# Kernel tuning notes

Measured on AMD Instinct MI355X. Metric: run time of the kernel, lower is better.

Reference implementation:

```python
import jax, jax.numpy as jnp
import numpy as np

DIM = 128
NUM_HEADS = 4
WH, WW = 7, 7
N = WH * WW            # 49 tokens per window
NW = 64                # number of windows (56/7)^2
BATCH = 64
B_ = BATCH * NW        # 4096


def _relative_position_index(Wh, Ww):
    coords = np.stack(np.meshgrid(np.arange(Wh), np.arange(Ww), indexing='ij'))  # [2,Wh,Ww]
    coords = coords.reshape(2, -1)
    rel = coords[:, :, None] - coords[:, None, :]          # [2, N, N]
    rel = rel.transpose(1, 2, 0).astype(np.int64)          # [N, N, 2]
    rel[:, :, 0] += Wh - 1
    rel[:, :, 1] += Ww - 1
    rel[:, :, 0] *= 2 * Ww - 1
    return rel.sum(-1)                                     # [N, N]


def setup_inputs() -> dict:
    key = jax.random.key(0)
    ks = jax.random.split(key, 8)
    x = jax.random.normal(ks[0], (B_, N, DIM), dtype=jnp.float32)
    # Swin shift-mask: additive, 0 or large negative; random floats are fine for math check
    mask = jax.random.normal(ks[1], (NW, N, N), dtype=jnp.float32)
    qkv_w = jax.random.normal(ks[2], (DIM, 3 * DIM), dtype=jnp.float32) * 0.02
    qkv_b = jax.random.normal(ks[3], (3 * DIM,), dtype=jnp.float32) * 0.02
    proj_w = jax.random.normal(ks[4], (DIM, DIM), dtype=jnp.float32) * 0.02
    proj_b = jax.random.normal(ks[5], (DIM,), dtype=jnp.float32) * 0.02
    table_size = (2 * WH - 1) * (2 * WW - 1)  # 169
    bias_table = jax.random.normal(ks[6], (table_size, NUM_HEADS), dtype=jnp.float32) * 0.02
    rel_idx = jnp.asarray(_relative_position_index(WH, WW), dtype=jnp.int32)  # [N,N]
    return {"x": x, "mask": mask, "qkv_w": qkv_w, "qkv_b": qkv_b,
            "proj_w": proj_w, "proj_b": proj_b, "bias_table": bias_table,
            "rel_idx": rel_idx}


def reference(x, mask, qkv_w, qkv_b, proj_w, proj_b, bias_table, rel_idx):
    B, Nn, C = x.shape
    H = bias_table.shape[1]
    hd = C // H
    scale = hd ** -0.5
    # qkv projection -> [3, B, H, N, hd]
    qkv = (x @ qkv_w + qkv_b).reshape(B, Nn, 3, H, hd).transpose(2, 0, 3, 1, 4)
    q, k, v = qkv[0] * scale, qkv[1], qkv[2]
    attn = jnp.einsum('bhnd,bhmd->bhnm', q, k)  # [B,H,N,N]
    # gathered relative position bias -> [H,N,N]
    bias = bias_table[rel_idx.reshape(-1)].reshape(Nn, Nn, H).transpose(2, 0, 1)
    attn = attn + bias[None]
    nW = mask.shape[0]
    attn = attn.reshape(-1, nW, H, Nn, Nn) + mask[None, :, None].astype(attn.dtype)
    attn = jax.nn.softmax(attn.reshape(-1, H, Nn, Nn), axis=-1)
    out = jnp.einsum('bhnm,bhmd->bnhd', attn, v).reshape(B, Nn, C)
    return out @ proj_w + proj_b
```

## Files before the change

### kernel.cpp

```cpp
#include <hip/hip_runtime.h>

#define NTOK 49
#define DIMC 128
#define NH   4
#define NWIN 64
#define NBLK 4096

#define WPROJ_OFF 98304
#define BMF_OFF   131072

typedef unsigned short u16x8 __attribute__((ext_vector_type(8)));
typedef __bf16        bf16x8 __attribute__((ext_vector_type(8)));
typedef float         f32x4  __attribute__((ext_vector_type(4)));

__device__ __forceinline__ unsigned short f2bf(float f) {
  return __builtin_bit_cast(unsigned short, (__bf16)f);
}

__device__ __forceinline__ bf16x8 ld_frag(const unsigned short* p) {
  return __builtin_bit_cast(bf16x8, *(const u16x8*)p);
}

__device__ __forceinline__ bf16x8 pack_bf16x8(float4 lo, float4 hi) {
  bf16x8 r;
  r[0] = (__bf16)lo.x; r[1] = (__bf16)lo.y; r[2] = (__bf16)lo.z; r[3] = (__bf16)lo.w;
  r[4] = (__bf16)hi.x; r[5] = (__bf16)hi.y; r[6] = (__bf16)hi.z; r[7] = (__bf16)hi.w;
  return r;
}

#define MFMA(a, b, c) __builtin_amdgcn_mfma_f32_16x16x32_bf16(a, b, c, 0, 0, 0)

__global__ void prep_kernel(const float* __restrict__ qkv_w,
                            const float* __restrict__ proj_w,
                            const float* __restrict__ bias_table,
                            const int*   __restrict__ rel_idx,
                            const float* __restrict__ mask,
                            unsigned short* __restrict__ wqkv,
                            unsigned short* __restrict__ wproj,
                            float* __restrict__ bmf)
{
  const int tid = blockIdx.x * blockDim.x + threadIdx.x;
  const int nth = gridDim.x * blockDim.x;

  for (int idx = tid; idx < 4*24*64*8; idx += nth) {
    int ii = idx & 7, lane = (idx >> 3) & 63, rest = idx >> 9;
    int ct = rest % 24, kt = rest / 24;
    int k = kt*32 + ((lane >> 4) << 3) + ii;
    int c = ct*16 + (lane & 15);
    wqkv[idx] = f2bf(qkv_w[k*384 + c]);
  }
  for (int idx = tid; idx < 4*8*64*8; idx += nth) {
    int ii = idx & 7, lane = (idx >> 3) & 63, rest = idx >> 9;
    int ct = rest & 7, kt = rest >> 3;
    int k = kt*32 + ((lane >> 4) << 3) + ii;
    int c = ct*16 + (lane & 15);
    wproj[idx] = f2bf(proj_w[k*128 + c]);
  }
  for (int idx = tid; idx < NWIN*NH*16*256; idx += nth) {
    int r2   = idx & 3;
    int lane = (idx >> 2) & 63;
    int ij   = (idx >> 8) & 15;
    int h    = (idx >> 12) & 3;
    int wi   = idx >> 14;
    int it = ij >> 2, jt = ij & 3;
    int q = jt*16 + (lane & 15);
    int k = it*16 + ((lane >> 4) << 2) + r2;
    float v = -1e30f;
    if (q < NTOK && k < NTOK)
      v = mask[wi*2401 + q*49 + k] + bias_table[rel_idx[q*49 + k]*4 + h];
    bmf[idx] = v;
  }
}

#define SLOT 6272
__global__ __launch_bounds__(256, 3) void winattn_kernel(
    const float* __restrict__ x,
    const float* __restrict__ qkv_b,
    const float* __restrict__ proj_b,
    const unsigned short* __restrict__ wqkv,
    const unsigned short* __restrict__ wproj,
    const float* __restrict__ bmf,
    float* __restrict__ out)
{
  __shared__ __align__(16) unsigned short smem[4*SLOT];

  const int b    = blockIdx.x;
  const int wi   = b & (NWIN - 1);
  const int tid  = threadIdx.x;
  const int h    = tid >> 6;
  const int lane = tid & 63;
  const int lhi  = lane >> 4;
  const int llo  = lane & 15;

  unsigned short* slot = smem + h*SLOT;
  unsigned short* Qh  = slot;
  unsigned short* Kh  = slot + 1764;
  unsigned short* Vh  = slot + 4096;
  unsigned short* Pb  = slot;
  unsigned short* XOh = slot;

  const f32x4 zv = {0.f, 0.f, 0.f, 0.f};
  const float* xb = x + (size_t)b * (NTOK*DIMC);

  f32x4 acc[6][4];
  #pragma unroll
  for (int j = 0; j < 6; j++)
    #pragma unroll
    for (int i = 0; i < 4; i++) acc[j][i] = zv;

  #pragma unroll
  for (int kt = 0; kt < 4; kt++) {
    bf16x8 a[4];
    #pragma unroll
    for (int i = 0; i < 4; i++) {
      float4 lo = make_float4(0.f,0.f,0.f,0.f), hi = lo;
      int row = i*16 + llo;
      if (i < 3 || row < NTOK) {
        const float4* p = (const float4*)(xb + row*DIMC + kt*32 + lhi*8);
        lo = p[0]; hi = p[1];
      }
      a[i] = pack_bf16x8(lo, hi);
    }
    #pragma unroll
    for (int j = 0; j < 6; j++) {
      int ct = (j >> 1)*8 + h*2 + (j & 1);
      bf16x8 bw = ld_frag(wqkv + (((kt*24 + ct)*64 + lane) << 3));
      #pragma unroll
      for (int i = 0; i < 4; i++) acc[j][i] = MFMA(a[i], bw, acc[j][i]);
    }
  }

  float bias[6];
  #pragma unroll
  for (int j = 0; j < 6; j++)
    bias[j] = qkv_b[((j >> 1)*8 + h*2 + (j & 1))*16 + llo];

  const float scale = 0.17677669529663687f;

  #pragma unroll
  for (int j = 0; j < 2; j++) {
    int d = j*16 + llo;
    #pragma unroll
    for (int i = 0; i < 4; i++)
      #pragma unroll
      for (int r2 = 0; r2 < 4; r2++) {
        int r = i*16 + lhi*4 + r2;
        if (r < NTOK) Qh[r*36 + d] = f2bf((acc[0+j][i][r2] + bias[j]) * scale);
      }
  }

  float4 bmv[16];
  {
    const float4* bmf4 = (const float4*)bmf + (size_t)(wi*4 + h)*16*64 + lane;
    #pragma unroll
    for (int t = 0; t < 16; t++) bmv[t] = bmf4[t*64];
  }

  #pragma unroll
  for (int j = 2; j < 4; j++) {
    int d = (j - 2)*16 + llo;
    #pragma unroll
    for (int i = 0; i < 4; i++)
      #pragma unroll
      for (int r2 = 0; r2 < 4; r2++) {
        int r = i*16 + lhi*4 + r2;
        if (r < NTOK) Kh[r*36 + d] = f2bf(acc[j][i][r2] + bias[j]);
      }
  }
  #pragma unroll
  for (int j = 4; j < 6; j++) {
    int d = (j - 4)*16 + llo;
    #pragma unroll
    for (int i = 0; i < 4; i++) {
      ushort4 pk;
      pk.x = f2bf(acc[j][i][0] + bias[j]);
      pk.y = f2bf(acc[j][i][1] + bias[j]);
      pk.z = f2bf(acc[j][i][2] + bias[j]);
      pk.w = f2bf(acc[j][i][3] + bias[j]);
      *(ushort4*)(Vh + d*68 + i*16 + lhi*4) = pk;
    }
  }

  f32x4 s[4][4];
  #pragma unroll
  for (int it = 0; it < 4; it++)
    #pragma unroll
    for (int jt = 0; jt < 4; jt++) s[it][jt] = zv;

  {
    bf16x8 ka[4], qb[4];
    #pragma unroll
    for (int it = 0; it < 4; it++) ka[it] = ld_frag(Kh + (it*16 + llo)*36 + lhi*8);
    #pragma unroll
    for (int jt = 0; jt < 4; jt++) qb[jt] = ld_frag(Qh + (jt*16 + llo)*36 + lhi*8);
    __builtin_amdgcn_s_setprio(1);
    #pragma unroll
    for (int jt = 0; jt < 4; jt++)
      #pragma unroll
      for (int it = 0; it < 4; it++)
        s[it][jt] = MFMA(ka[it], qb[jt], s[it][jt]);
    __builtin_amdgcn_s_setprio(0);
  }

  #pragma unroll
  for (int jt = 0; jt < 4; jt++) {
    float e[4][4];
    float psum = 0.f;
    #pragma unroll
    for (int it = 0; it < 3; it++) {
      float4 t = bmv[it*4 + jt];
      #pragma unroll
      for (int r2 = 0; r2 < 4; r2++) {
        float v = __expf(s[it][jt][r2] + (&t.x)[r2]);
        e[it][r2] = v;
        psum += v;
      }
    }
    {
      float v = (lhi == 0) ? __expf(s[3][jt][0] + bmv[12 + jt].x) : 0.f;
      e[3][0] = v; e[3][1] = 0.f; e[3][2] = 0.f; e[3][3] = 0.f;
      psum += v;
    }
    psum += __shfl_xor(psum, 16, 64);
    psum += __shfl_xor(psum, 32, 64);
    float inv = __builtin_amdgcn_rcpf(psum);
    int q = jt*16 + llo;
    #pragma unroll
    for (int it = 0; it < 4; it++) {
      ushort4 pk;
      pk.x = f2bf(e[it][0] * inv);
      pk.y = f2bf(e[it][1] * inv);
      pk.z = f2bf(e[it][2] * inv);
      pk.w = f2bf(e[it][3] * inv);
      int el = (q*64 + it*16 + lhi*4) ^ ((llo & 7) << 3);
      *(ushort4*)(Pb + el) = pk;
    }
  }

  f32x4 o[2][4];
  #pragma unroll
  for (int mt = 0; mt < 2; mt++)
    #pragma unroll
    for (int nt = 0; nt < 4; nt++) o[mt][nt] = zv;

  #pragma unroll
  for (int ks = 0; ks < 2; ks++) {
    bf16x8 va[2], pbf[4];
    #pragma unroll
    for (int mt = 0; mt < 2; mt++)
      va[mt] = ld_frag(Vh + (mt*16 + llo)*68 + ks*32 + lhi*8);
    #pragma unroll
    for (int nt = 0; nt < 4; nt++) {
      int el = ((nt*16 + llo)*64 + ks*32 + lhi*8) ^ ((llo & 7) << 3);
      pbf[nt] = ld_frag(Pb + el);
    }
    __builtin_amdgcn_s_setprio(1);
    #pragma unroll
    for (int nt = 0; nt < 4; nt++)
      #pragma unroll
      for (int mt = 0; mt < 2; mt++)
        o[mt][nt] = MFMA(va[mt], pbf[nt], o[mt][nt]);
    __builtin_amdgcn_s_setprio(0);
  }

  #pragma unroll
  for (int nt = 0; nt < 4; nt++) {
    int q = nt*16 + llo;
    if (q < NTOK) {
      #pragma unroll
      for (int mt = 0; mt < 2; mt++) {
        ushort4 pk;
        pk.x = f2bf(o[mt][nt][0]);
        pk.y = f2bf(o[mt][nt][1]);
        pk.z = f2bf(o[mt][nt][2]);
        pk.w = f2bf(o[mt][nt][3]);
        *(ushort4*)(XOh + q*36 + mt*16 + lhi*4) = pk;
      }
    }
  }

  __syncthreads();

  {
    f32x4 pacc[2][4];
    #pragma unroll
    for (int j = 0; j < 2; j++)
      #pragma unroll
      for (int i = 0; i < 4; i++) pacc[j][i] = zv;

    #pragma unroll
    for (int kt = 0; kt < 4; kt++) {
      bf16x8 a[4];
      #pragma unroll
      for (int i = 0; i < 4; i++)
        a[i] = ld_frag(smem + kt*SLOT + (i*16 + llo)*36 + lhi*8);
      #pragma unroll
      for (int j = 0; j < 2; j++) {
        int ct = h*2 + j;
        bf16x8 bw = ld_frag(wproj + (((kt*8 + ct)*64 + lane) << 3));
        #pragma unroll
        for (int i = 0; i < 4; i++) pacc[j][i] = MFMA(a[i], bw, pacc[j][i]);
      }
    }

    float* op = out + (size_t)b * (NTOK*DIMC);
    #pragma unroll
    for (int j = 0; j < 2; j++) {
      int c = (h*2 + j)*16 + llo;
      float pb = proj_b[c];
      #pragma unroll
      for (int i = 0; i < 4; i++)
        #pragma unroll
        for (int r2 = 0; r2 < 4; r2++) {
          int r = i*16 + lhi*4 + r2;
          if (r < NTOK) op[r*128 + c] = pacc[j][i][r2] + pb;
        }
    }
  }
}

extern "C" void kernel_launch(void* const* d_in, const int* in_sizes, int n_in,
                              void* d_out, int out_size, void* d_ws, size_t ws_size,
                              hipStream_t stream)
{
  const float* x          = (const float*)d_in[0];
  const float* mask       = (const float*)d_in[1];
  const float* qkv_w      = (const float*)d_in[2];
  const float* qkv_b      = (const float*)d_in[3];
  const float* proj_w     = (const float*)d_in[4];
  const float* proj_b     = (const float*)d_in[5];
  const float* bias_table = (const float*)d_in[6];
  const int*   rel_idx    = (const int*)d_in[7];
  float* out = (float*)d_out;

  unsigned short* wqkv  = (unsigned short*)d_ws;
  unsigned short* wproj = (unsigned short*)((char*)d_ws + WPROJ_OFF);
  float*          bmf   = (float*)((char*)d_ws + BMF_OFF);

  prep_kernel<<<1024, 256, 0, stream>>>(qkv_w, proj_w, bias_table, rel_idx, mask,
                                        wqkv, wproj, bmf);
  winattn_kernel<<<NBLK, 256, 0, stream>>>(x, qkv_b, proj_b, wqkv, wproj, bmf, out);
}
```

Measured before the change: 113.1 us.

## Split each head across two waves with 512-thread blocks

Doubles the block to 8 waves so each head is handled by two waves. Each wave computes half the token row tiles in the QKV projection, half the query tiles in attention and PV, and one 16-column tile of the output projection. The goal is to cut per-wave register pressure and serial MFMA chains and to expose more parallelism per window. In exchange it adds block-wide barriers (QKV staging now needs one before attention, plus one before the XO writes) and moves XO to a separate LDS offset. Occupancy changes with the new launch bounds.

```diff
diff --git a/kernel.cpp b/kernel.cpp
--- a/kernel.cpp
+++ b/kernel.cpp
@@ -73,7 +73,7 @@
 }
 
 #define SLOT 6272
-__global__ __launch_bounds__(256, 3) void winattn_kernel(
+__global__ __launch_bounds__(512, 3) void winattn_kernel(
     const float* __restrict__ x,
     const float* __restrict__ qkv_b,
     const float* __restrict__ proj_b,
@@ -87,7 +87,9 @@
   const int b    = blockIdx.x;
   const int wi   = b & (NWIN - 1);
   const int tid  = threadIdx.x;
-  const int h    = tid >> 6;
+  const int wave = tid >> 6;
+  const int h    = wave & 3;
+  const int ws   = wave >> 2;
   const int lane = tid & 63;
   const int lhi  = lane >> 4;
   const int llo  = lane & 15;
@@ -97,36 +99,34 @@
   unsigned short* Kh  = slot + 1764;
   unsigned short* Vh  = slot + 4096;
   unsigned short* Pb  = slot;
-  unsigned short* XOh = slot;
+  unsigned short* XOh = slot + 2048;
 
   const f32x4 zv = {0.f, 0.f, 0.f, 0.f};
   const float* xb = x + (size_t)b * (NTOK*DIMC);
 
-  f32x4 acc[6][4];
-  #pragma unroll
-  for (int j = 0; j < 6; j++)
-    #pragma unroll
-    for (int i = 0; i < 4; i++) acc[j][i] = zv;
+  f32x4 acc[6][2];
+  #pragma unroll
+  for (int j = 0; j < 6; j++) { acc[j][0] = zv; acc[j][1] = zv; }
 
   #pragma unroll
   for (int kt = 0; kt < 4; kt++) {
-    bf16x8 a[4];
-    #pragma unroll
-    for (int i = 0; i < 4; i++) {
+    bf16x8 a[2];
+    #pragma unroll
+    for (int il = 0; il < 2; il++) {
+      int row = (ws*2 + il)*16 + llo;
       float4 lo = make_float4(0.f,0.f,0.f,0.f), hi = lo;
-      int row = i*16 + llo;
-      if (i < 3 || row < NTOK) {
+      if (ws == 0 || row < NTOK) {
         const float4* p = (const float4*)(xb + row*DIMC + kt*32 + lhi*8);
         lo = p[0]; hi = p[1];
       }
-      a[i] = pack_bf16x8(lo, hi);
+      a[il] = pack_bf16x8(lo, hi);
     }
     #pragma unroll
     for (int j = 0; j < 6; j++) {
       int ct = (j >> 1)*8 + h*2 + (j & 1);
       bf16x8 bw = ld_frag(wqkv + (((kt*24 + ct)*64 + lane) << 3));
       #pragma unroll
-      for (int i = 0; i < 4; i++) acc[j][i] = MFMA(a[i], bw, acc[j][i]);
+      for (int il = 0; il < 2; il++) acc[j][il] = MFMA(a[il], bw, acc[j][il]);
     }
   }
 
@@ -141,90 +141,103 @@
   for (int j = 0; j < 2; j++) {
     int d = j*16 + llo;
     #pragma unroll
-    for (int i = 0; i < 4; i++)
+    for (int il = 0; il < 2; il++)
       #pragma unroll
       for (int r2 = 0; r2 < 4; r2++) {
-        int r = i*16 + lhi*4 + r2;
-        if (r < NTOK) Qh[r*36 + d] = f2bf((acc[0+j][i][r2] + bias[j]) * scale);
-      }
-  }
-
-  float4 bmv[16];
+        int r = (ws*2 + il)*16 + lhi*4 + r2;
+        if (r < NTOK) Qh[r*36 + d] = f2bf((acc[j][il][r2] + bias[j]) * scale);
+      }
+  }
+
+  float4 bmv[8];
   {
     const float4* bmf4 = (const float4*)bmf + (size_t)(wi*4 + h)*16*64 + lane;
     #pragma unroll
-    for (int t = 0; t < 16; t++) bmv[t] = bmf4[t*64];
+    for (int it = 0; it < 4; it++)
+      #pragma unroll
+      for (int jtl = 0; jtl < 2; jtl++)
+        bmv[it*2 + jtl] = bmf4[(it*4 + ws*2 + jtl)*64];
   }
 
   #pragma unroll
   for (int j = 2; j < 4; j++) {
     int d = (j - 2)*16 + llo;
     #pragma unroll
-    for (int i = 0; i < 4; i++)
+    for (int il = 0; il < 2; il++)
       #pragma unroll
       for (int r2 = 0; r2 < 4; r2++) {
-        int r = i*16 + lhi*4 + r2;
-        if (r < NTOK) Kh[r*36 + d] = f2bf(acc[j][i][r2] + bias[j]);
+        int r = (ws*2 + il)*16 + lhi*4 + r2;
+        if (r < NTOK) Kh[r*36 + d] = f2bf(acc[j][il][r2] + bias[j]);
       }
   }
   #pragma unroll
   for (int j = 4; j < 6; j++) {
     int d = (j - 4)*16 + llo;
     #pragma unroll
-    for (int i = 0; i < 4; i++) {
+    for (int il = 0; il < 2; il++) {
       ushort4 pk;
-      pk.x = f2bf(acc[j][i][0] + bias[j]);
-      pk.y = f2bf(acc[j][i][1] + bias[j]);
-      pk.z = f2bf(acc[j][i][2] + bias[j]);
-      pk.w = f2bf(acc[j][i][3] + bias[j]);
-      *(ushort4*)(Vh + d*68 + i*16 + lhi*4) = pk;
-    }
-  }
-
-  f32x4 s[4][4];
-  #pragma unroll
-  for (int it = 0; it < 4; it++)
-    #pragma unroll
-    for (int jt = 0; jt < 4; jt++) s[it][jt] = zv;
+      pk.x = f2bf(acc[j][il][0] + bias[j]);
+      pk.y = f2bf(acc[j][il][1] + bias[j]);
+      pk.z = f2bf(acc[j][il][2] + bias[j]);
+      pk.w = f2bf(acc[j][il][3] + bias[j]);
+      *(ushort4*)(Vh + d*68 + (ws*2 + il)*16 + lhi*4) = pk;
+    }
+  }
+
+  __syncthreads();
+
+  f32x4 s[4][2];
+  #pragma unroll
+  for (int it = 0; it < 4; it++) { s[it][0] = zv; s[it][1] = zv; }
 
   {
-    bf16x8 ka[4], qb[4];
+    bf16x8 ka[4], qb[2];
     #pragma unroll
     for (int it = 0; it < 4; it++) ka[it] = ld_frag(Kh + (it*16 + llo)*36 + lhi*8);
     #pragma unroll
-    for (int jt = 0; jt < 4; jt++) qb[jt] = ld_frag(Qh + (jt*16 + llo)*36 + lhi*8);
+    for (int jtl = 0; jtl < 2; jtl++)
+      qb[jtl] = ld_frag(Qh + ((ws*2 + jtl)*16 + llo)*36 + lhi*8);
     __builtin_amdgcn_s_setprio(1);
     #pragma unroll
-    for (int jt = 0; jt < 4; jt++)
+    for (int jtl = 0; jtl < 2; jtl++)
       #pragma unroll
       for (int it = 0; it < 4; it++)
-        s[it][jt] = MFMA(ka[it], qb[jt], s[it][jt]);
+        s[it][jtl] = MFMA(ka[it], qb[jtl], s[it][jtl]);
     __builtin_amdgcn_s_setprio(0);
   }
 
   #pragma unroll
-  for (int jt = 0; jt < 4; jt++) {
+  for (int jtl = 0; jtl < 2; jtl++) {
+    #pragma unroll
+    for (int it = 0; it < 3; it++) {
+      float4 t = bmv[it*2 + jtl];
+      #pragma unroll
+      for (int r2 = 0; r2 < 4; r2++) s[it][jtl][r2] += (&t.x)[r2];
+    }
+    s[3][jtl][0] += bmv[6 + jtl].x;
+  }
+
+  #pragma unroll
+  for (int jtl = 0; jtl < 2; jtl++) {
     float e[4][4];
     float psum = 0.f;
     #pragma unroll
-    for (int it = 0; it < 3; it++) {
-      float4 t = bmv[it*4 + jt];
+    for (int it = 0; it < 3; it++)
       #pragma unroll
       for (int r2 = 0; r2 < 4; r2++) {
-        float v = __expf(s[it][jt][r2] + (&t.x)[r2]);
+        float v = __expf(s[it][jtl][r2]);
         e[it][r2] = v;
         psum += v;
       }
-    }
     {
-      float v = (lhi == 0) ? __expf(s[3][jt][0] + bmv[12 + jt].x) : 0.f;
+      float v = (lhi == 0) ? __expf(s[3][jtl][0]) : 0.f;
       e[3][0] = v; e[3][1] = 0.f; e[3][2] = 0.f; e[3][3] = 0.f;
       psum += v;
     }
     psum += __shfl_xor(psum, 16, 64);
     psum += __shfl_xor(psum, 32, 64);
     float inv = __builtin_amdgcn_rcpf(psum);
-    int q = jt*16 + llo;
+    int q = (ws*2 + jtl)*16 + llo;
     #pragma unroll
     for (int it = 0; it < 4; it++) {
       ushort4 pk;
@@ -237,43 +250,42 @@
     }
   }
 
-  f32x4 o[2][4];
-  #pragma unroll
-  for (int mt = 0; mt < 2; mt++)
-    #pragma unroll
-    for (int nt = 0; nt < 4; nt++) o[mt][nt] = zv;
+  f32x4 o[2][2];
+  o[0][0] = zv; o[0][1] = zv; o[1][0] = zv; o[1][1] = zv;
 
   #pragma unroll
   for (int ks = 0; ks < 2; ks++) {
-    bf16x8 va[2], pbf[4];
+    bf16x8 va[2], pbf[2];
     #pragma unroll
     for (int mt = 0; mt < 2; mt++)
       va[mt] = ld_frag(Vh + (mt*16 + llo)*68 + ks*32 + lhi*8);
     #pragma unroll
-    for (int nt = 0; nt < 4; nt++) {
-      int el = ((nt*16 + llo)*64 + ks*32 + lhi*8) ^ ((llo & 7) << 3);
-      pbf[nt] = ld_frag(Pb + el);
+    for (int jtl = 0; jtl < 2; jtl++) {
+      int el = (((ws*2 + jtl)*16 + llo)*64 + ks*32 + lhi*8) ^ ((llo & 7) << 3);
+      pbf[jtl] = ld_frag(Pb + el);
     }
     __builtin_amdgcn_s_setprio(1);
     #pragma unroll
-    for (int nt = 0; nt < 4; nt++)
+    for (int jtl = 0; jtl < 2; jtl++)
       #pragma unroll
       for (int mt = 0; mt < 2; mt++)
-        o[mt][nt] = MFMA(va[mt], pbf[nt], o[mt][nt]);
+        o[mt][jtl] = MFMA(va[mt], pbf[jtl], o[mt][jtl]);
     __builtin_amdgcn_s_setprio(0);
   }
 
-  #pragma unroll
-  for (int nt = 0; nt < 4; nt++) {
-    int q = nt*16 + llo;
+  __syncthreads();
+
+  #pragma unroll
+  for (int jtl = 0; jtl < 2; jtl++) {
+    int q = (ws*2 + jtl)*16 + llo;
     if (q < NTOK) {
       #pragma unroll
       for (int mt = 0; mt < 2; mt++) {
         ushort4 pk;
-        pk.x = f2bf(o[mt][nt][0]);
-        pk.y = f2bf(o[mt][nt][1]);
-        pk.z = f2bf(o[mt][nt][2]);
-        pk.w = f2bf(o[mt][nt][3]);
+        pk.x = f2bf(o[mt][jtl][0]);
+        pk.y = f2bf(o[mt][jtl][1]);
+        pk.z = f2bf(o[mt][jtl][2]);
+        pk.w = f2bf(o[mt][jtl][3]);
         *(ushort4*)(XOh + q*36 + mt*16 + lhi*4) = pk;
       }
     }
@@ -282,40 +294,31 @@
   __syncthreads();
 
   {
-    f32x4 pacc[2][4];
-    #pragma unroll
-    for (int j = 0; j < 2; j++)
-      #pragma unroll
-      for (int i = 0; i < 4; i++) pacc[j][i] = zv;
+    f32x4 pacc[4];
+    #pragma unroll
+    for (int i = 0; i < 4; i++) pacc[i] = zv;
 
     #pragma unroll
     for (int kt = 0; kt < 4; kt++) {
       bf16x8 a[4];
       #pragma unroll
       for (int i = 0; i < 4; i++)
-        a[i] = ld_frag(smem + kt*SLOT + (i*16 + llo)*36 + lhi*8);
-      #pragma unroll
-      for (int j = 0; j < 2; j++) {
-        int ct = h*2 + j;
-        bf16x8 bw = ld_frag(wproj + (((kt*8 + ct)*64 + lane) << 3));
-        #pragma unroll
-        for (int i = 0; i < 4; i++) pacc[j][i] = MFMA(a[i], bw, pacc[j][i]);
-      }
+        a[i] = ld_frag(smem + kt*SLOT + 2048 + (i*16 + llo)*36 + lhi*8);
+      bf16x8 bw = ld_frag(wproj + (((kt*8 + wave)*64 + lane) << 3));
+      #pragma unroll
+      for (int i = 0; i < 4; i++) pacc[i] = MFMA(a[i], bw, pacc[i]);
     }
 
     float* op = out + (size_t)b * (NTOK*DIMC);
-    #pragma unroll
-    for (int j = 0; j < 2; j++) {
-      int c = (h*2 + j)*16 + llo;
-      float pb = proj_b[c];
-      #pragma unroll
-      for (int i = 0; i < 4; i++)
-        #pragma unroll
-        for (int r2 = 0; r2 < 4; r2++) {
-          int r = i*16 + lhi*4 + r2;
-          if (r < NTOK) op[r*128 + c] = pacc[j][i][r2] + pb;
-        }
-    }
+    int c = wave*16 + llo;
+    float pb = proj_b[c];
+    #pragma unroll
+    for (int i = 0; i < 4; i++)
+      #pragma unroll
+      for (int r2 = 0; r2 < 4; r2++) {
+        int r = i*16 + lhi*4 + r2;
+        if (r < NTOK) op[r*128 + c] = pacc[i][r2] + pb;
+      }
   }
 }
 
@@ -339,5 +342,5 @@
 
   prep_kernel<<<1024, 256, 0, stream>>>(qkv_w, proj_w, bias_table, rel_idx, mask,
                                         wqkv, wproj, bmf);
-  winattn_kernel<<<NBLK, 256, 0, stream>>>(x, qkv_b, proj_b, wqkv, wproj, bmf, out);
-}
+  winattn_kernel<<<NBLK, 512, 0, stream>>>(x, qkv_b, proj_b, wqkv, wproj, bmf, out);
+}
```

After: 152.0 us. +34.4%, slower.

## Stage bf16 input tile in LDS once and share across head waves

Applied to the files above, without the earlier changes.

Before, each of the four head waves loaded the full fp32 x tile from global memory and converted it to bf16 itself, so every x element was read four times. Now the block loads x once cooperatively, converts it to bf16 into a shared LDS tile, and each wave reads its MFMA A fragments from there. The LDS layout is repartitioned so the x tile and V share a region that is only reused after a new barrier, which adds two __syncthreads. The gain is less global traffic and conversion work, at the cost of extra synchronisation and LDS reads.

```diff
diff --git a/kernel.cpp b/kernel.cpp
--- a/kernel.cpp
+++ b/kernel.cpp
@@ -19,13 +19,6 @@
 
 __device__ __forceinline__ bf16x8 ld_frag(const unsigned short* p) {
   return __builtin_bit_cast(bf16x8, *(const u16x8*)p);
-}
-
-__device__ __forceinline__ bf16x8 pack_bf16x8(float4 lo, float4 hi) {
-  bf16x8 r;
-  r[0] = (__bf16)lo.x; r[1] = (__bf16)lo.y; r[2] = (__bf16)lo.z; r[3] = (__bf16)lo.w;
-  r[4] = (__bf16)hi.x; r[5] = (__bf16)hi.y; r[6] = (__bf16)hi.z; r[7] = (__bf16)hi.w;
-  return r;
 }
 
 #define MFMA(a, b, c) __builtin_amdgcn_mfma_f32_16x16x32_bf16(a, b, c, 0, 0, 0)
@@ -72,7 +65,6 @@
   }
 }
 
-#define SLOT 6272
 __global__ __launch_bounds__(256, 3) void winattn_kernel(
     const float* __restrict__ x,
     const float* __restrict__ qkv_b,
@@ -82,7 +74,7 @@
     const float* __restrict__ bmf,
     float* __restrict__ out)
 {
-  __shared__ __align__(16) unsigned short smem[4*SLOT];
+  __shared__ __align__(16) unsigned short smem[25088];
 
   const int b    = blockIdx.x;
   const int wi   = b & (NWIN - 1);
@@ -92,16 +84,32 @@
   const int lhi  = lane >> 4;
   const int llo  = lane & 15;
 
-  unsigned short* slot = smem + h*SLOT;
-  unsigned short* Qh  = slot;
-  unsigned short* Kh  = slot + 1764;
-  unsigned short* Vh  = slot + 4096;
-  unsigned short* Pb  = slot;
-  unsigned short* XOh = slot;
+  unsigned short* reg = smem + h*4096;
+  unsigned short* Qh  = reg;
+  unsigned short* Kh  = reg + 1764;
+  unsigned short* Pb  = reg;
+  unsigned short* XOh = reg;
+  unsigned short* xs  = smem + 16384;
+  unsigned short* Vh  = smem + 16384 + h*2176;
 
   const f32x4 zv = {0.f, 0.f, 0.f, 0.f};
   const float* xb = x + (size_t)b * (NTOK*DIMC);
 
+  {
+    const float4* xv = (const float4*)xb;
+    #pragma unroll
+    for (int t = 0; t < 8; t++) {
+      int idx = t*256 + tid;
+      int n = idx >> 5, c4 = idx & 31;
+      float4 v = make_float4(0.f, 0.f, 0.f, 0.f);
+      if (n < NTOK) v = xv[n*32 + c4];
+      ushort4 pk;
+      pk.x = f2bf(v.x); pk.y = f2bf(v.y); pk.z = f2bf(v.z); pk.w = f2bf(v.w);
+      *(ushort4*)(xs + n*136 + c4*4) = pk;
+    }
+  }
+  __syncthreads();
+
   f32x4 acc[6][4];
   #pragma unroll
   for (int j = 0; j < 6; j++)
@@ -112,15 +120,8 @@
   for (int kt = 0; kt < 4; kt++) {
     bf16x8 a[4];
     #pragma unroll
-    for (int i = 0; i < 4; i++) {
-      float4 lo = make_float4(0.f,0.f,0.f,0.f), hi = lo;
-      int row = i*16 + llo;
-      if (i < 3 || row < NTOK) {
-        const float4* p = (const float4*)(xb + row*DIMC + kt*32 + lhi*8);
-        lo = p[0]; hi = p[1];
-      }
-      a[i] = pack_bf16x8(lo, hi);
-    }
+    for (int i = 0; i < 4; i++)
+      a[i] = ld_frag(xs + (i*16 + llo)*136 + kt*32 + lhi*8);
     #pragma unroll
     for (int j = 0; j < 6; j++) {
       int ct = (j >> 1)*8 + h*2 + (j & 1);
@@ -145,7 +146,18 @@
       #pragma unroll
       for (int r2 = 0; r2 < 4; r2++) {
         int r = i*16 + lhi*4 + r2;
-        if (r < NTOK) Qh[r*36 + d] = f2bf((acc[0+j][i][r2] + bias[j]) * scale);
+        if (r < NTOK) Qh[r*36 + d] = f2bf((acc[j][i][r2] + bias[j]) * scale);
+      }
+  }
+  #pragma unroll
+  for (int j = 2; j < 4; j++) {
+    int d = (j - 2)*16 + llo;
+    #pragma unroll
+    for (int i = 0; i < 4; i++)
+      #pragma unroll
+      for (int r2 = 0; r2 < 4; r2++) {
+        int r = i*16 + lhi*4 + r2;
+        if (r < NTOK) Kh[r*36 + d] = f2bf(acc[j][i][r2] + bias[j]);
       }
   }
 
@@ -156,17 +168,8 @@
     for (int t = 0; t < 16; t++) bmv[t] = bmf4[t*64];
   }
 
-  #pragma unroll
-  for (int j = 2; j < 4; j++) {
-    int d = (j - 2)*16 + llo;
-    #pragma unroll
-    for (int i = 0; i < 4; i++)
-      #pragma unroll
-      for (int r2 = 0; r2 < 4; r2++) {
-        int r = i*16 + lhi*4 + r2;
-        if (r < NTOK) Kh[r*36 + d] = f2bf(acc[j][i][r2] + bias[j]);
-      }
-  }
+  __syncthreads();
+
   #pragma unroll
   for (int j = 4; j < 6; j++) {
     int d = (j - 4)*16 + llo;
@@ -293,7 +296,7 @@
       bf16x8 a[4];
       #pragma unroll
       for (int i = 0; i < 4; i++)
-        a[i] = ld_frag(smem + kt*SLOT + (i*16 + llo)*36 + lhi*8);
+        a[i] = ld_frag(smem + kt*4096 + (i*16 + llo)*36 + lhi*8);
       #pragma unroll
       for (int j = 0; j < 2; j++) {
         int ct = h*2 + j;
```

Result: faster. 104.6 us (-7.5%).
